# Optimization experiments

Measured on AMD Instinct MI355X. Metric: run time of the kernel, lower is better.

## Reference

```python
import jax, jax.numpy as jnp
import numpy as np

B, S, HID = 1, 2048, 2048   # batch, block_size, hidden_dim
H, D = 16, 128              # num_heads, head_dim
WORLD_SIZE = 4
LOCAL_BLOCK_IDX = 3         # last rank: all kv blocks are causally visible


def setup_inputs() -> dict:
    key = jax.random.key(0)
    ks = jax.random.split(key, 5)
    w = lambda k: jax.random.normal(k, (H * D, HID), dtype=jnp.float32) * 0.02
    return {
        "hidden_states": jax.random.normal(ks[0], (B, S, HID), dtype=jnp.float32),
        "q_w": w(ks[1]), "q_b": jnp.zeros((H * D,), jnp.float32),
        "k_w": w(ks[2]), "k_b": jnp.zeros((H * D,), jnp.float32),
        "v_w": w(ks[3]), "v_b": jnp.zeros((H * D,), jnp.float32),
        "o_w": jax.random.normal(ks[4], (HID, H * D), dtype=jnp.float32) * 0.02,
        "o_b": jnp.zeros((HID,), jnp.float32),
        "world_size": WORLD_SIZE,
        "local_block_idx": LOCAL_BLOCK_IDX,
    }


def reference(hidden_states, q_w, q_b, k_w, k_b, v_w, v_b, o_w, o_b,
              world_size, local_block_idx):
    Bsz, Sq, _ = hidden_states.shape

    def proj(w, b):  # (B,S,HID) -> (B,H,S,D)
        return (hidden_states @ w.T + b).reshape(Bsz, Sq, H, D).transpose(0, 2, 1, 3)

    q, k, v = proj(q_w, q_b), proj(k_w, k_b), proj(v_w, v_b)
    scale = D ** -0.5

    # ring_send_recv is a local copy, so K/V are identical every ring step;
    # only the causal masking differs (triu mask on the diagonal block step).
    scores_base = jnp.einsum('bhqd,bhkd->bhqk', q, k) * scale
    tri = jnp.triu(jnp.ones((Sq, Sq), bool), k=1)
    scores_diag = jnp.where(tri, -jnp.inf, scores_base)

    out = jnp.zeros((Bsz, H, Sq, D), hidden_states.dtype)
    mx = jnp.full((Bsz, H, Sq, 1), -jnp.inf, hidden_states.dtype)
    se = jnp.zeros((Bsz, H, Sq, 1), hidden_states.dtype)

    for step in range(world_size):  # small fixed ring loop
        kv_idx = (local_block_idx - step) % world_size
        scores = scores_diag if kv_idx == local_block_idx else scores_base
        # OnlineSoftmax.update (faithful, including block-wise normalization)
        bm = scores.max(axis=-1, keepdims=True)
        nm = jnp.maximum(mx, bm)
        old_s = jnp.exp(mx - nm)
        new_s = jnp.exp(bm - nm)
        be = jnp.exp(scores - bm)
        bs = be.sum(axis=-1, keepdims=True)
        se = se * old_s + bs * new_s
        aw = be / (bs + 1e-8)
        bo = jnp.einsum('bhqk,bhkd->bhqd', aw, v)
        out = out * old_s + bo * new_s
        mx = nm

    out = out / (se + 1e-8)  # OnlineSoftmax.finalize
    out = out.transpose(0, 2, 1, 3).reshape(Bsz, Sq, H * D)
    return out @ o_w.T + o_b
```

## Files before the change

kernel.cpp:

```cpp
#include <hip/hip_runtime.h>
#include <hip/hip_bf16.h>
#include <stdint.h>
#include <stddef.h>


typedef __attribute__((ext_vector_type(8))) short bf16x8;
typedef __attribute__((ext_vector_type(4))) float f32x4;

#define MFMA_BF16(a, b, c) __builtin_amdgcn_mfma_f32_16x16x32_bf16((a), (b), (c), 0, 0, 0)

__device__ __forceinline__ void load16_lds(const void* g, void* l) {
  __builtin_amdgcn_global_load_lds((const __attribute__((address_space(1))) void*)g,
                                   (__attribute__((address_space(3))) void*)l,
                                   16, 0, 0);
}

__device__ __forceinline__ unsigned short f2bf(float x) {
  union { __hip_bfloat16 b; unsigned short u; } cv;
  cv.b = __float2bfloat16(x);
  return cv.u;
}

__global__ __launch_bounds__(256) void cvt_all(
    const float4* __restrict__ s0, const float4* __restrict__ s1,
    const float4* __restrict__ s2, const float4* __restrict__ s3,
    const float4* __restrict__ s4,
    ushort4* __restrict__ d0, ushort4* __restrict__ d1,
    ushort4* __restrict__ d2, ushort4* __restrict__ d3,
    ushort4* __restrict__ d4) {
  const int seg = blockIdx.x >> 12;
  const int i = ((blockIdx.x & 4095) << 8) + threadIdx.x;
  const float4* s = seg == 0 ? s0 : seg == 1 ? s1 : seg == 2 ? s2 : seg == 3 ? s3 : s4;
  ushort4* d = seg == 0 ? d0 : seg == 1 ? d1 : seg == 2 ? d2 : seg == 3 ? d3 : d4;
  float4 v = s[i];
  ushort4 o;
  o.x = f2bf(v.x); o.y = f2bf(v.y); o.z = f2bf(v.z); o.w = f2bf(v.w);
  d[i] = o;
}

__global__ __launch_bounds__(256) void gemm_qkv(
    const unsigned short* __restrict__ A, const unsigned short* __restrict__ Bt,
    const float* __restrict__ qb, const float* __restrict__ kb,
    const float* __restrict__ vb,
    unsigned short* __restrict__ Qo, unsigned short* __restrict__ Ko,
    unsigned short* __restrict__ Vt) {
  __shared__ __align__(16) unsigned short sA[128 * 64];
  __shared__ __align__(16) unsigned short sB[128 * 64];
  const int tid = threadIdx.x;
  const int wave = tid >> 6, lane = tid & 63;
  const int quad = lane >> 4, l16 = lane & 15;
  const int wr = wave >> 1, wc = wave & 1;
  const int m0 = blockIdx.y << 7, n0 = blockIdx.x << 7;

  f32x4 acc[4][4] = {};

  for (int k0 = 0; k0 < 2048; k0 += 64) {
    __syncthreads();
#pragma unroll
    for (int t = 0; t < 4; t++) {
      const int i = t * 4 + wave;
      const int idx = i * 64 + lane;
      const int row = idx >> 3;
      const int c = (idx & 7) ^ (row & 7);
      load16_lds(A + (size_t)(m0 + row) * 2048 + k0 + c * 8, &sA[i * 512]);
      load16_lds(Bt + (size_t)(n0 + row) * 2048 + k0 + c * 8, &sB[i * 512]);
    }
    __syncthreads();
#pragma unroll
    for (int ks = 0; ks < 2; ks++) {
      bf16x8 af[4], bfr[4];
#pragma unroll
      for (int i = 0; i < 4; i++) {
        const int cs = ((ks * 4 + quad) ^ (l16 & 7)) << 3;
        af[i] = *(const bf16x8*)&sA[(wr * 64 + i * 16 + l16) * 64 + cs];
        bfr[i] = *(const bf16x8*)&sB[(wc * 64 + i * 16 + l16) * 64 + cs];
      }
#pragma unroll
      for (int mi = 0; mi < 4; mi++)
#pragma unroll
        for (int ni = 0; ni < 4; ni++)
          acc[mi][ni] = MFMA_BF16(af[mi], bfr[ni], acc[mi][ni]);
    }
  }

  const float qscale = 0.088388347648318447f * 1.4426950408889634f;
#pragma unroll
  for (int mi = 0; mi < 4; mi++) {
    const int row = m0 + wr * 64 + mi * 16 + quad * 4;
#pragma unroll
    for (int ni = 0; ni < 4; ni++) {
      const int col = n0 + wc * 64 + ni * 16 + l16;
#pragma unroll
      for (int r = 0; r < 4; r++) {
        const float v = acc[mi][ni][r];
        const int rr = row + r;
        if (col < 2048) {
          const int hh = col >> 7, d = col & 127;
          Qo[((size_t)hh * 2048 + rr) * 128 + d] = f2bf((v + qb[col]) * qscale);
        } else if (col < 4096) {
          const int f = col - 2048;
          const int hh = f >> 7, d = f & 127;
          Ko[((size_t)hh * 2048 + rr) * 128 + d] = f2bf(v + kb[f]);
        } else {
          const int f = col - 4096;
          const int hh = f >> 7, d = f & 127;
          Vt[((size_t)hh * 128 + d) * 2048 + rr] = f2bf(v + vb[f]);
        }
      }
    }
  }
}

__global__ __launch_bounds__(256) void attn_fwd(
    const unsigned short* __restrict__ Q, const unsigned short* __restrict__ K,
    const unsigned short* __restrict__ V,
    unsigned short* __restrict__ O,
    const int* __restrict__ wsp) {
  const int h = blockIdx.y;
  const int q0 = blockIdx.x << 6;
  const int tid = threadIdx.x;
  const int wave = tid >> 6, lane = tid & 63;
  const int quad = lane >> 4, l16 = lane & 15;

  __shared__ __align__(16) unsigned short sQ[64 * 128];
  __shared__ __align__(16) unsigned short sK[64 * 128];
  __shared__ __align__(16) unsigned short sV[128 * 64];
  __shared__ __align__(16) unsigned short sP[4][16 * 64];

  const unsigned short* Qh = Q + (size_t)h * 2048 * 128;
  const unsigned short* Kh = K + (size_t)h * 2048 * 128;
  const unsigned short* Vh = V + (size_t)h * 128 * 2048;
  unsigned short* sPw = sP[wave];

  for (int c = wave; c < 16; c += 4) {
    const int rowc = lane >> 4;
    const int row = c * 4 + rowc;
    const int blk = (lane & 15) ^ (row & 15);
    load16_lds(Qh + (size_t)(q0 + row) * 128 + blk * 8, &sQ[c * 512]);
  }
  __syncthreads();

  bf16x8 qf[4];
#pragma unroll
  for (int ds = 0; ds < 4; ds++)
    qf[ds] = *(const bf16x8*)&sQ[(wave * 16 + l16) * 128 + (((ds * 4 + quad) ^ l16) << 3)];

  float m1 = -3.0e38f, l1 = 0.f, m2 = -3.0e38f, l2 = 0.f;
  f32x4 o1[8], o2[8];
#pragma unroll
  for (int j = 0; j < 8; j++) { o1[j] = f32x4{0.f, 0.f, 0.f, 0.f}; o2[j] = f32x4{0.f, 0.f, 0.f, 0.f}; }

  const int diag = q0 >> 6;
  const int qg = q0 + wave * 16 + l16;

  auto update = [&](float& m, float& l, f32x4 (&o)[8],
                    const f32x4 (&st)[4], bool masked, int k0) {
    float t[4][4];
    float mx = -3.0e38f;
#pragma unroll
    for (int ni = 0; ni < 4; ni++)
#pragma unroll
      for (int r = 0; r < 4; r++) {
        float v = st[ni][r];
        if (masked && (k0 + ni * 16 + quad * 4 + r > qg)) v = -3.0e38f;
        t[ni][r] = v;
        mx = fmaxf(mx, v);
      }
    mx = fmaxf(mx, __shfl_xor(mx, 16));
    mx = fmaxf(mx, __shfl_xor(mx, 32));
    const float mn = fmaxf(m, mx);
    const float al = exp2f(m - mn);
    float rs = 0.f;
#pragma unroll
    for (int ni = 0; ni < 4; ni++) {
      union { unsigned short u[4]; uint2 v; } pk;
#pragma unroll
      for (int r = 0; r < 4; r++) {
        const float p = exp2f(t[ni][r] - mn);
        rs += p;
        pk.u[r] = f2bf(p);
      }
      const int off = l16 * 64 + (((ni * 2 + (quad >> 1)) ^ (l16 & 7)) << 3) + ((quad & 1) << 2);
      *(uint2*)&sPw[off] = pk.v;
    }
    rs += __shfl_xor(rs, 16);
    rs += __shfl_xor(rs, 32);
    l = l * al + rs;
    m = mn;
#pragma unroll
    for (int r = 0; r < 4; r++) {
      const int src = (lane & 48) + ((lane >> 4) << 2) + r;
      const float ab = __shfl(al, src);
#pragma unroll
      for (int j = 0; j < 8; j++) o[j][r] *= ab;
    }
#pragma unroll
    for (int ks = 0; ks < 2; ks++) {
      const bf16x8 pf = *(const bf16x8*)&sPw[l16 * 64 + (((ks * 4 + quad) ^ (l16 & 7)) << 3)];
#pragma unroll
      for (int j = 0; j < 8; j++) {
        const bf16x8 vf =
            *(const bf16x8*)&sV[(j * 16 + l16) * 64 + (((ks * 4 + quad) ^ (l16 & 7)) << 3)];
        o[j] = MFMA_BF16(pf, vf, o[j]);
      }
    }
  };

  for (int kt = 0; kt < 32; kt++) {
    const int k0 = kt << 6;
    __syncthreads();
    for (int c = wave; c < 16; c += 4) {
      {
        const int rowc = lane >> 4;
        const int row = c * 4 + rowc;
        const int blk = (lane & 15) ^ (row & 15);
        load16_lds(Kh + (size_t)(k0 + row) * 128 + blk * 8, &sK[c * 512]);
      }
      {
        const int rowc = lane >> 3;
        const int row = c * 8 + rowc;
        const int blk = (lane & 7) ^ (rowc & 7);
        load16_lds(Vh + (size_t)row * 2048 + k0 + blk * 8, &sV[c * 512]);
      }
    }
    __syncthreads();

    f32x4 st[4];
#pragma unroll
    for (int ni = 0; ni < 4; ni++) st[ni] = f32x4{0.f, 0.f, 0.f, 0.f};
#pragma unroll
    for (int ds = 0; ds < 4; ds++) {
#pragma unroll
      for (int ni = 0; ni < 4; ni++) {
        const bf16x8 kf =
            *(const bf16x8*)&sK[(ni * 16 + l16) * 128 + (((ds * 4 + quad) ^ l16) << 3)];
        st[ni] = MFMA_BF16(kf, qf[ds], st[ni]);
      }
    }

    if (kt == diag) {
      m1 = m2; l1 = l2;
#pragma unroll
      for (int j = 0; j < 8; j++) o1[j] = o2[j];
      update(m1, l1, o1, st, true, k0);
    }
    update(m2, l2, o2, st, false, k0);
  }

  const float fws = (float)(wsp[0] - 1);
  const float a = exp2f(m1 - m2);
  const float se = l1 * a + fws * l2;
  const float inv = 1.0f / (se + 1e-8f);
  const float f1 = (a / (l1 + 1e-8f)) * inv;
  const float f2 = (fws / (l2 + 1e-8f)) * inv;
#pragma unroll
  for (int r = 0; r < 4; r++) {
    const int src = (lane & 48) + ((lane >> 4) << 2) + r;
    const float f1b = __shfl(f1, src);
    const float f2b = __shfl(f2, src);
    const int row = q0 + wave * 16 + quad * 4 + r;
#pragma unroll
    for (int j = 0; j < 8; j++) {
      const float ov = o1[j][r] * f1b + o2[j][r] * f2b;
      O[(size_t)row * 2048 + h * 128 + j * 16 + l16] = f2bf(ov);
    }
  }
}

__global__ __launch_bounds__(256) void gemm_o(
    const unsigned short* __restrict__ A, const unsigned short* __restrict__ Bt,
    const float* __restrict__ ob, float* __restrict__ Cout) {
  __shared__ __align__(16) unsigned short sA[64 * 64];
  __shared__ __align__(16) unsigned short sB[128 * 64];
  const int tid = threadIdx.x;
  const int wave = tid >> 6, lane = tid & 63;
  const int quad = lane >> 4, l16 = lane & 15;
  const int wm = wave >> 1, wn = wave & 1;
  const int m0 = blockIdx.y << 6, n0 = blockIdx.x << 7;

  f32x4 acc[2][4] = {};

  for (int k0 = 0; k0 < 2048; k0 += 64) {
    __syncthreads();
#pragma unroll
    for (int t = 0; t < 2; t++) {
      const int i = t * 4 + wave;
      const int idx = i * 64 + lane;
      const int row = idx >> 3;
      const int c = (idx & 7) ^ (row & 7);
      load16_lds(A + (size_t)(m0 + row) * 2048 + k0 + c * 8, &sA[i * 512]);
    }
#pragma unroll
    for (int t = 0; t < 4; t++) {
      const int i = t * 4 + wave;
      const int idx = i * 64 + lane;
      const int row = idx >> 3;
      const int c = (idx & 7) ^ (row & 7);
      load16_lds(Bt + (size_t)(n0 + row) * 2048 + k0 + c * 8, &sB[i * 512]);
    }
    __syncthreads();
#pragma unroll
    for (int ks = 0; ks < 2; ks++) {
      const int cs = ((ks * 4 + quad) ^ (l16 & 7)) << 3;
      bf16x8 af[2], bfr[4];
#pragma unroll
      for (int i = 0; i < 2; i++)
        af[i] = *(const bf16x8*)&sA[(wm * 32 + i * 16 + l16) * 64 + cs];
#pragma unroll
      for (int i = 0; i < 4; i++)
        bfr[i] = *(const bf16x8*)&sB[(wn * 64 + i * 16 + l16) * 64 + cs];
#pragma unroll
      for (int mi = 0; mi < 2; mi++)
#pragma unroll
        for (int ni = 0; ni < 4; ni++)
          acc[mi][ni] = MFMA_BF16(af[mi], bfr[ni], acc[mi][ni]);
    }
  }

#pragma unroll
  for (int mi = 0; mi < 2; mi++) {
    const int row = m0 + wm * 32 + mi * 16 + quad * 4;
#pragma unroll
    for (int ni = 0; ni < 4; ni++) {
      const int col = n0 + wn * 64 + ni * 16 + l16;
#pragma unroll
      for (int r = 0; r < 4; r++) {
        Cout[(size_t)(row + r) * 2048 + col] = acc[mi][ni][r] + ob[col];
      }
    }
  }
}

extern "C" void kernel_launch(void* const* d_in, const int* in_sizes, int n_in,
                              void* d_out, int out_size, void* d_ws, size_t ws_size,
                              hipStream_t stream) {
  (void)in_sizes; (void)n_in; (void)out_size; (void)ws_size;
  const float* hs = (const float*)d_in[0];
  const float* qw = (const float*)d_in[1];
  const float* qb = (const float*)d_in[2];
  const float* kw = (const float*)d_in[3];
  const float* kb = (const float*)d_in[4];
  const float* vw = (const float*)d_in[5];
  const float* vb = (const float*)d_in[6];
  const float* ow = (const float*)d_in[7];
  const float* ob = (const float*)d_in[8];
  const int* wsz = (const int*)d_in[9];

  char* w = (char*)d_ws;
  unsigned short* hsb  = (unsigned short*)(w + 0);
  unsigned short* wqkv = (unsigned short*)(w + 8388608);
  unsigned short* owb  = (unsigned short*)(w + 33554432);
  unsigned short* Qb_  = (unsigned short*)(w + 41943040);
  unsigned short* Kb_  = (unsigned short*)(w + 50331648);
  unsigned short* Vtb  = (unsigned short*)(w + 58720256);
  unsigned short* atb  = (unsigned short*)(w + 67108864);

  cvt_all<<<20480, 256, 0, stream>>>(
      (const float4*)hs, (const float4*)qw, (const float4*)kw, (const float4*)vw,
      (const float4*)ow,
      (ushort4*)hsb, (ushort4*)wqkv, (ushort4*)(wqkv + 4194304),
      (ushort4*)(wqkv + 8388608), (ushort4*)owb);

  gemm_qkv<<<dim3(48, 16), 256, 0, stream>>>(hsb, wqkv, qb, kb, vb, Qb_, Kb_, Vtb);
  attn_fwd<<<dim3(32, 16), 256, 0, stream>>>(Qb_, Kb_, Vtb, atb, wsz);
  gemm_o<<<dim3(16, 32), 256, 0, stream>>>(atb, owb, ob, (float*)d_out);
}
```

Measured before the change: 334.7 us.

## Split attention KV range across blocks with merge kernel and widen gemm_o K tile

After: 417.2 us. 1.25x slower.

```diff
diff --git a/kernel.cpp b/kernel.cpp
--- a/kernel.cpp
+++ b/kernel.cpp
@@ -19,6 +19,11 @@
   union { __hip_bfloat16 b; unsigned short u; } cv;
   cv.b = __float2bfloat16(x);
   return cv.u;
+}
+__device__ __forceinline__ float bf2f(unsigned short u) {
+  union { unsigned int i; float f; } cv;
+  cv.i = ((unsigned int)u) << 16;
+  return cv.f;
 }
 
 __global__ __launch_bounds__(256) void cvt_all(
@@ -111,57 +116,66 @@
   }
 }
 
-__global__ __launch_bounds__(256) void attn_fwd(
+__global__ __launch_bounds__(128, 2) void attn_fwd(
     const unsigned short* __restrict__ Q, const unsigned short* __restrict__ K,
     const unsigned short* __restrict__ V,
-    unsigned short* __restrict__ O,
-    const int* __restrict__ wsp) {
-  const int h = blockIdx.y;
-  const int q0 = blockIdx.x << 6;
+    unsigned short* __restrict__ oU, unsigned short* __restrict__ oM,
+    float* __restrict__ stats) {
+  const int qt = blockIdx.x, kr = blockIdx.y, h = blockIdx.z;
+  const int b = (h * 2 + kr) * 32 + qt;
   const int tid = threadIdx.x;
   const int wave = tid >> 6, lane = tid & 63;
   const int quad = lane >> 4, l16 = lane & 15;
 
-  __shared__ __align__(16) unsigned short sQ[64 * 128];
-  __shared__ __align__(16) unsigned short sK[64 * 128];
+  __shared__ __align__(16) unsigned short sQK[64 * 128];
   __shared__ __align__(16) unsigned short sV[128 * 64];
-  __shared__ __align__(16) unsigned short sP[4][16 * 64];
+  __shared__ __align__(16) unsigned short sP[2 * 2 * 1024];
 
   const unsigned short* Qh = Q + (size_t)h * 2048 * 128;
   const unsigned short* Kh = K + (size_t)h * 2048 * 128;
   const unsigned short* Vh = V + (size_t)h * 128 * 2048;
-  unsigned short* sPw = sP[wave];
-
-  for (int c = wave; c < 16; c += 4) {
+
+  for (int c = wave; c < 16; c += 2) {
     const int rowc = lane >> 4;
     const int row = c * 4 + rowc;
     const int blk = (lane & 15) ^ (row & 15);
-    load16_lds(Qh + (size_t)(q0 + row) * 128 + blk * 8, &sQ[c * 512]);
+    load16_lds(Qh + (size_t)(qt * 64 + row) * 128 + blk * 8, &sQK[c * 512]);
   }
   __syncthreads();
 
-  bf16x8 qf[4];
-#pragma unroll
-  for (int ds = 0; ds < 4; ds++)
-    qf[ds] = *(const bf16x8*)&sQ[(wave * 16 + l16) * 128 + (((ds * 4 + quad) ^ l16) << 3)];
-
-  float m1 = -3.0e38f, l1 = 0.f, m2 = -3.0e38f, l2 = 0.f;
-  f32x4 o1[8], o2[8];
-#pragma unroll
-  for (int j = 0; j < 8; j++) { o1[j] = f32x4{0.f, 0.f, 0.f, 0.f}; o2[j] = f32x4{0.f, 0.f, 0.f, 0.f}; }
-
-  const int diag = q0 >> 6;
-  const int qg = q0 + wave * 16 + l16;
-
-  auto update = [&](float& m, float& l, f32x4 (&o)[8],
-                    const f32x4 (&st)[4], bool masked, int k0) {
+  bf16x8 qf[2][4];
+#pragma unroll
+  for (int s = 0; s < 2; s++)
+#pragma unroll
+    for (int ds = 0; ds < 4; ds++)
+      qf[s][ds] = *(const bf16x8*)&sQK[(wave * 32 + s * 16 + l16) * 128 +
+                                       (((ds * 4 + quad) ^ l16) << 3)];
+
+  float m1[2] = {-3.0e38f, -3.0e38f}, l1[2] = {0.f, 0.f};
+  float m2[2] = {-3.0e38f, -3.0e38f}, l2[2] = {0.f, 0.f};
+  f32x4 o1[2][8], o2[2][8];
+#pragma unroll
+  for (int s = 0; s < 2; s++)
+#pragma unroll
+    for (int j = 0; j < 8; j++) {
+      o1[s][j] = f32x4{0.f, 0.f, 0.f, 0.f};
+      o2[s][j] = f32x4{0.f, 0.f, 0.f, 0.f};
+    }
+
+  const int kbase = kr << 10;
+  const int dloc = qt - (kr << 4);
+  const bool inrange = (qt >> 4) == kr;
+
+  auto softmax_update = [&](int sub, float& m, float& l, f32x4 (&o)[8],
+                            const f32x4 (&stt)[4], bool masked, int k0) {
+    const int qg = qt * 64 + wave * 32 + sub * 16 + l16;
     float t[4][4];
     float mx = -3.0e38f;
 #pragma unroll
     for (int ni = 0; ni < 4; ni++)
 #pragma unroll
       for (int r = 0; r < 4; r++) {
-        float v = st[ni][r];
+        float v = stt[ni][r];
         if (masked && (k0 + ni * 16 + quad * 4 + r > qg)) v = -3.0e38f;
         t[ni][r] = v;
         mx = fmaxf(mx, v);
@@ -170,6 +184,7 @@
     mx = fmaxf(mx, __shfl_xor(mx, 32));
     const float mn = fmaxf(m, mx);
     const float al = exp2f(m - mn);
+    unsigned short* sPw = &sP[(wave * 2 + sub) * 1024];
     float rs = 0.f;
 #pragma unroll
     for (int ni = 0; ni < 4; ni++) {
@@ -180,7 +195,8 @@
         rs += p;
         pk.u[r] = f2bf(p);
       }
-      const int off = l16 * 64 + (((ni * 2 + (quad >> 1)) ^ (l16 & 7)) << 3) + ((quad & 1) << 2);
+      const int off =
+          l16 * 64 + (((ni * 2 + (quad >> 1)) ^ (l16 & 7)) << 3) + ((quad & 1) << 2);
       *(uint2*)&sPw[off] = pk.v;
     }
     rs += __shfl_xor(rs, 16);
@@ -189,32 +205,37 @@
     m = mn;
 #pragma unroll
     for (int r = 0; r < 4; r++) {
-      const int src = (lane & 48) + ((lane >> 4) << 2) + r;
+      const int src = (lane & 48) + quad * 4 + r;
       const float ab = __shfl(al, src);
 #pragma unroll
       for (int j = 0; j < 8; j++) o[j][r] *= ab;
     }
+  };
+
+  auto pv_shared = [&](f32x4 (&oo)[2][8]) {
 #pragma unroll
     for (int ks = 0; ks < 2; ks++) {
-      const bf16x8 pf = *(const bf16x8*)&sPw[l16 * 64 + (((ks * 4 + quad) ^ (l16 & 7)) << 3)];
+      const int cs = (((ks * 4 + quad) ^ (l16 & 7)) << 3);
+      const bf16x8 pf0 = *(const bf16x8*)&sP[(wave * 2 + 0) * 1024 + l16 * 64 + cs];
+      const bf16x8 pf1 = *(const bf16x8*)&sP[(wave * 2 + 1) * 1024 + l16 * 64 + cs];
 #pragma unroll
       for (int j = 0; j < 8; j++) {
-        const bf16x8 vf =
-            *(const bf16x8*)&sV[(j * 16 + l16) * 64 + (((ks * 4 + quad) ^ (l16 & 7)) << 3)];
-        o[j] = MFMA_BF16(pf, vf, o[j]);
+        const bf16x8 vf = *(const bf16x8*)&sV[(j * 16 + l16) * 64 + cs];
+        oo[0][j] = MFMA_BF16(pf0, vf, oo[0][j]);
+        oo[1][j] = MFMA_BF16(pf1, vf, oo[1][j]);
       }
     }
   };
 
-  for (int kt = 0; kt < 32; kt++) {
-    const int k0 = kt << 6;
-    __syncthreads();
-    for (int c = wave; c < 16; c += 4) {
+  for (int kt = 0; kt < 16; kt++) {
+    const int k0 = kbase + (kt << 6);
+    __syncthreads();
+    for (int c = wave; c < 16; c += 2) {
       {
         const int rowc = lane >> 4;
         const int row = c * 4 + rowc;
         const int blk = (lane & 15) ^ (row & 15);
-        load16_lds(Kh + (size_t)(k0 + row) * 128 + blk * 8, &sK[c * 512]);
+        load16_lds(Kh + (size_t)(k0 + row) * 128 + blk * 8, &sQK[c * 512]);
       }
       {
         const int rowc = lane >> 3;
@@ -225,27 +246,92 @@
     }
     __syncthreads();
 
-    f32x4 st[4];
-#pragma unroll
-    for (int ni = 0; ni < 4; ni++) st[ni] = f32x4{0.f, 0.f, 0.f, 0.f};
+    f32x4 st[2][4];
+#pragma unroll
+    for (int s = 0; s < 2; s++)
+#pragma unroll
+      for (int ni = 0; ni < 4; ni++) st[s][ni] = f32x4{0.f, 0.f, 0.f, 0.f};
 #pragma unroll
     for (int ds = 0; ds < 4; ds++) {
 #pragma unroll
       for (int ni = 0; ni < 4; ni++) {
         const bf16x8 kf =
-            *(const bf16x8*)&sK[(ni * 16 + l16) * 128 + (((ds * 4 + quad) ^ l16) << 3)];
-        st[ni] = MFMA_BF16(kf, qf[ds], st[ni]);
-      }
-    }
-
-    if (kt == diag) {
-      m1 = m2; l1 = l2;
-#pragma unroll
-      for (int j = 0; j < 8; j++) o1[j] = o2[j];
-      update(m1, l1, o1, st, true, k0);
-    }
-    update(m2, l2, o2, st, false, k0);
-  }
+            *(const bf16x8*)&sQK[(ni * 16 + l16) * 128 + (((ds * 4 + quad) ^ l16) << 3)];
+        st[0][ni] = MFMA_BF16(kf, qf[0][ds], st[0][ni]);
+        st[1][ni] = MFMA_BF16(kf, qf[1][ds], st[1][ni]);
+      }
+    }
+
+    if (inrange && kt == dloc) {
+#pragma unroll
+      for (int s = 0; s < 2; s++) {
+        m1[s] = m2[s]; l1[s] = l2[s];
+#pragma unroll
+        for (int j = 0; j < 8; j++) o1[s][j] = o2[s][j];
+      }
+      softmax_update(0, m1[0], l1[0], o1[0], st[0], true, k0);
+      softmax_update(1, m1[1], l1[1], o1[1], st[1], true, k0);
+      pv_shared(o1);
+    }
+    softmax_update(0, m2[0], l2[0], o2[0], st[0], false, k0);
+    softmax_update(1, m2[1], l2[1], o2[1], st[1], false, k0);
+    pv_shared(o2);
+  }
+
+  if (!inrange && kr == 0) {
+#pragma unroll
+    for (int s = 0; s < 2; s++) {
+      m1[s] = m2[s]; l1[s] = l2[s];
+#pragma unroll
+      for (int j = 0; j < 8; j++) o1[s][j] = o2[s][j];
+    }
+  }
+
+#pragma unroll
+  for (int s = 0; s < 2; s++) {
+    if (quad == 0) {
+      const int q = wave * 32 + s * 16 + l16;
+      stats[b * 64 + q] = m2[s];
+      stats[65536 + b * 64 + q] = l2[s];
+      stats[131072 + b * 64 + q] = m1[s];
+      stats[196608 + b * 64 + q] = l1[s];
+    }
+#pragma unroll
+    for (int j = 0; j < 8; j++)
+#pragma unroll
+      for (int r = 0; r < 4; r++) {
+        const int q = wave * 32 + s * 16 + quad * 4 + r;
+        const int d = j * 16 + l16;
+        const size_t idx = ((size_t)b * 64 + q) * 128 + d;
+        oU[idx] = f2bf(o2[s][j][r]);
+        oM[idx] = f2bf(o1[s][j][r]);
+      }
+  }
+}
+
+__global__ __launch_bounds__(256) void attn_merge(
+    const unsigned short* __restrict__ oU, const unsigned short* __restrict__ oM,
+    const float* __restrict__ stats, unsigned short* __restrict__ atb,
+    const int* __restrict__ wsp) {
+  const int tid = blockIdx.x * 256 + threadIdx.x;
+  const int d8 = tid & 15;
+  const int q = (tid >> 4) & 2047;
+  const int h = tid >> 15;
+  const int qt = q >> 6, qloc = q & 63;
+  const int b0 = (h * 2 + 0) * 32 + qt;
+  const int b1 = (h * 2 + 1) * 32 + qt;
+
+  const float mU0 = stats[b0 * 64 + qloc], mU1 = stats[b1 * 64 + qloc];
+  const float lU0 = stats[65536 + b0 * 64 + qloc], lU1 = stats[65536 + b1 * 64 + qloc];
+  const float mM0 = stats[131072 + b0 * 64 + qloc], mM1 = stats[131072 + b1 * 64 + qloc];
+  const float lM0 = stats[196608 + b0 * 64 + qloc], lM1 = stats[196608 + b1 * 64 + qloc];
+
+  const float m2 = fmaxf(mU0, mU1);
+  const float e0 = exp2f(mU0 - m2), e1 = exp2f(mU1 - m2);
+  const float l2 = lU0 * e0 + lU1 * e1;
+  const float m1 = fmaxf(mM0, mM1);
+  const float g0 = exp2f(mM0 - m1), g1 = exp2f(mM1 - m1);
+  const float l1 = lM0 * g0 + lM1 * g1;
 
   const float fws = (float)(wsp[0] - 1);
   const float a = exp2f(m1 - m2);
@@ -253,25 +339,39 @@
   const float inv = 1.0f / (se + 1e-8f);
   const float f1 = (a / (l1 + 1e-8f)) * inv;
   const float f2 = (fws / (l2 + 1e-8f)) * inv;
-#pragma unroll
-  for (int r = 0; r < 4; r++) {
-    const int src = (lane & 48) + ((lane >> 4) << 2) + r;
-    const float f1b = __shfl(f1, src);
-    const float f2b = __shfl(f2, src);
-    const int row = q0 + wave * 16 + quad * 4 + r;
-#pragma unroll
-    for (int j = 0; j < 8; j++) {
-      const float ov = o1[j][r] * f1b + o2[j][r] * f2b;
-      O[(size_t)row * 2048 + h * 128 + j * 16 + l16] = f2bf(ov);
-    }
-  }
+
+  const size_t i0 = ((size_t)b0 * 64 + qloc) * 128 + d8 * 8;
+  const size_t i1 = ((size_t)b1 * 64 + qloc) * 128 + d8 * 8;
+  const ushort4* pU0 = (const ushort4*)(oU + i0);
+  const ushort4* pU1 = (const ushort4*)(oU + i1);
+  const ushort4* pM0 = (const ushort4*)(oM + i0);
+  const ushort4* pM1 = (const ushort4*)(oM + i1);
+
+  union { unsigned short u[8]; ushort4 v[2]; } out;
+#pragma unroll
+  for (int half = 0; half < 2; half++) {
+    const ushort4 u0 = pU0[half], u1 = pU1[half], w0 = pM0[half], w1 = pM1[half];
+    const unsigned short* a0 = (const unsigned short*)&u0;
+    const unsigned short* a1 = (const unsigned short*)&u1;
+    const unsigned short* c0 = (const unsigned short*)&w0;
+    const unsigned short* c1 = (const unsigned short*)&w1;
+#pragma unroll
+    for (int k = 0; k < 4; k++) {
+      const float ov2 = bf2f(a0[k]) * e0 + bf2f(a1[k]) * e1;
+      const float ov1 = bf2f(c0[k]) * g0 + bf2f(c1[k]) * g1;
+      out.u[half * 4 + k] = f2bf(ov1 * f1 + ov2 * f2);
+    }
+  }
+  ushort4* dst = (ushort4*)(atb + (size_t)q * 2048 + h * 128 + d8 * 8);
+  dst[0] = out.v[0];
+  dst[1] = out.v[1];
 }
 
 __global__ __launch_bounds__(256) void gemm_o(
     const unsigned short* __restrict__ A, const unsigned short* __restrict__ Bt,
     const float* __restrict__ ob, float* __restrict__ Cout) {
-  __shared__ __align__(16) unsigned short sA[64 * 64];
-  __shared__ __align__(16) unsigned short sB[128 * 64];
+  __shared__ __align__(16) unsigned short sA[64 * 128];
+  __shared__ __align__(16) unsigned short sB[128 * 128];
   const int tid = threadIdx.x;
   const int wave = tid >> 6, lane = tid & 63;
   const int quad = lane >> 4, l16 = lane & 15;
@@ -280,35 +380,35 @@
 
   f32x4 acc[2][4] = {};
 
-  for (int k0 = 0; k0 < 2048; k0 += 64) {
-    __syncthreads();
-#pragma unroll
-    for (int t = 0; t < 2; t++) {
-      const int i = t * 4 + wave;
-      const int idx = i * 64 + lane;
-      const int row = idx >> 3;
-      const int c = (idx & 7) ^ (row & 7);
-      load16_lds(A + (size_t)(m0 + row) * 2048 + k0 + c * 8, &sA[i * 512]);
-    }
+  for (int k0 = 0; k0 < 2048; k0 += 128) {
+    __syncthreads();
 #pragma unroll
     for (int t = 0; t < 4; t++) {
       const int i = t * 4 + wave;
       const int idx = i * 64 + lane;
-      const int row = idx >> 3;
-      const int c = (idx & 7) ^ (row & 7);
+      const int row = idx >> 4;
+      const int c = (idx & 15) ^ (row & 15);
+      load16_lds(A + (size_t)(m0 + row) * 2048 + k0 + c * 8, &sA[i * 512]);
+    }
+#pragma unroll
+    for (int t = 0; t < 8; t++) {
+      const int i = t * 4 + wave;
+      const int idx = i * 64 + lane;
+      const int row = idx >> 4;
+      const int c = (idx & 15) ^ (row & 15);
       load16_lds(Bt + (size_t)(n0 + row) * 2048 + k0 + c * 8, &sB[i * 512]);
     }
     __syncthreads();
 #pragma unroll
-    for (int ks = 0; ks < 2; ks++) {
-      const int cs = ((ks * 4 + quad) ^ (l16 & 7)) << 3;
+    for (int ks = 0; ks < 4; ks++) {
+      const int cs = ((ks * 4 + quad) ^ l16) << 3;
       bf16x8 af[2], bfr[4];
 #pragma unroll
       for (int i = 0; i < 2; i++)
-        af[i] = *(const bf16x8*)&sA[(wm * 32 + i * 16 + l16) * 64 + cs];
+        af[i] = *(const bf16x8*)&sA[(wm * 32 + i * 16 + l16) * 128 + cs];
 #pragma unroll
       for (int i = 0; i < 4; i++)
-        bfr[i] = *(const bf16x8*)&sB[(wn * 64 + i * 16 + l16) * 64 + cs];
+        bfr[i] = *(const bf16x8*)&sB[(wn * 64 + i * 16 + l16) * 128 + cs];
 #pragma unroll
       for (int mi = 0; mi < 2; mi++)
 #pragma unroll
@@ -349,11 +449,14 @@
   char* w = (char*)d_ws;
   unsigned short* hsb  = (unsigned short*)(w + 0);
   unsigned short* wqkv = (unsigned short*)(w + 8388608);
+  unsigned short* oU   = (unsigned short*)(w + 0);
+  unsigned short* oM   = (unsigned short*)(w + 16777216);
   unsigned short* owb  = (unsigned short*)(w + 33554432);
   unsigned short* Qb_  = (unsigned short*)(w + 41943040);
   unsigned short* Kb_  = (unsigned short*)(w + 50331648);
   unsigned short* Vtb  = (unsigned short*)(w + 58720256);
   unsigned short* atb  = (unsigned short*)(w + 67108864);
+  float*          stp  = (float*)(w + 75497472);
 
   cvt_all<<<20480, 256, 0, stream>>>(
       (const float4*)hs, (const float4*)qw, (const float4*)kw, (const float4*)vw,
@@ -362,6 +465,7 @@
       (ushort4*)(wqkv + 8388608), (ushort4*)owb);
 
   gemm_qkv<<<dim3(48, 16), 256, 0, stream>>>(hsb, wqkv, qb, kb, vb, Qb_, Kb_, Vtb);
-  attn_fwd<<<dim3(32, 16), 256, 0, stream>>>(Qb_, Kb_, Vtb, atb, wsz);
+  attn_fwd<<<dim3(32, 2, 16), 128, 0, stream>>>(Qb_, Kb_, Vtb, oU, oM, stp);
+  attn_merge<<<2048, 256, 0, stream>>>(oU, oM, stp, atb, wsz);
   gemm_o<<<dim3(16, 32), 256, 0, stream>>>(atb, owb, ob, (float*)d_out);
 }
```
